# Optimization experiments

Hardware: AMD Instinct MI355X
Metric: run time of the kernel (lower is better)

## Reference

```python
import jax, jax.numpy as jnp
import numpy as np

# dims
B, D, H, W, C = 8, 16, 56, 56, 96
WD, WH, WW = 2, 7, 7          # window size (depth, height, width)
SD, SH, SW = 1, 3, 3          # shift size
NH = 3                        # num heads
HD = C // NH                  # head dim = 32
N = WD * WH * WW              # tokens per window = 98
NW = (D // WD) * (H // WH) * (W // WW)  # windows per image = 512
HIDDEN = 4 * C
EPS = 1e-5
TABLE = (2 * WD - 1) * (2 * WH - 1) * (2 * WW - 1)  # 507


def _rel_pos_index():
    # Faithful replica of get_relative_position_index (note the nonstandard
    # meshgrid argument order: width, depth, height with indexing='ij').
    yy, zz, xx = np.meshgrid(np.arange(WW), np.arange(WD), np.arange(WH), indexing='ij')
    coords = np.stack([zz, yy, xx]).reshape(3, -1)          # [3, N]
    rel = coords[:, :, None] - coords[:, None, :]           # [3, N, N]
    rel = rel.transpose(1, 2, 0)
    z = (rel[..., 0] + WD - 1) * (2 * WH - 1) * (2 * WW - 1)
    x = (rel[..., 1] + WH - 1) * (2 * WW - 1)
    y = rel[..., 2] + WW - 1
    return (z + x + y).astype(np.int32)                     # [N, N], values < 507


def _attn_mask():
    # Standard shifted-window mask: label 3x3x3 regions, -100 where labels differ.
    img = np.zeros((D, H, W), dtype=np.int32)
    cnt = 0
    for ds in (slice(0, -WD), slice(-WD, -SD), slice(-SD, None)):
        for hs in (slice(0, -WH), slice(-WH, -SH), slice(-SH, None)):
            for ws in (slice(0, -WW), slice(-WW, -SW), slice(-SW, None)):
                img[ds, hs, ws] = cnt
                cnt += 1
    mw = img.reshape(D // WD, WD, H // WH, WH, W // WW, WW)
    mw = mw.transpose(0, 2, 4, 1, 3, 5).reshape(NW, N)
    diff = mw[:, None, :] - mw[:, :, None]
    return np.where(diff != 0, np.float32(-100.0), np.float32(0.0))  # [NW, N, N]


def setup_inputs() -> dict:
    key = jax.random.key(0)
    ks = jax.random.split(key, 12)
    s = 0.02
    return {
        "x": jax.random.normal(ks[0], (B, D, H, W, C), jnp.float32),
        "mask_matrix": jnp.asarray(_attn_mask()),
        "g1": jnp.ones((C,), jnp.float32),
        "b1": jnp.zeros((C,), jnp.float32),
        "w_qkv": jax.random.normal(ks[1], (C, 3 * C), jnp.float32) * s,
        "b_qkv": jnp.zeros((3 * C,), jnp.float32),
        "w_proj": jax.random.normal(ks[2], (C, C), jnp.float32) * s,
        "b_proj": jnp.zeros((C,), jnp.float32),
        "bias_table": jax.random.normal(ks[3], (TABLE, NH), jnp.float32) * s,
        "rel_index": jnp.asarray(_rel_pos_index()),
        "g2": jnp.ones((C,), jnp.float32),
        "b2": jnp.zeros((C,), jnp.float32),
        "w_fc1": jax.random.normal(ks[4], (C, HIDDEN), jnp.float32) * s,
        "b_fc1": jnp.zeros((HIDDEN,), jnp.float32),
        "w_fc2": jax.random.normal(ks[5], (HIDDEN, C), jnp.float32) * s,
        "b_fc2": jnp.zeros((C,), jnp.float32),
    }


def _layernorm(x, g, b):
    mu = jnp.mean(x, axis=-1, keepdims=True)
    var = jnp.var(x, axis=-1, keepdims=True)
    return (x - mu) * jax.lax.rsqrt(var + EPS) * g + b


def reference(x, mask_matrix, g1, b1, w_qkv, b_qkv, w_proj, b_proj,
              bias_table, rel_index, g2, b2, w_fc1, b_fc1, w_fc2, b_fc2):
    shortcut = x
    h = _layernorm(x, g1, b1)
    # cyclic shift (no padding needed: dims divisible by window)
    h = jnp.roll(h, shift=(-SD, -SH, -SW), axis=(1, 2, 3))
    # window partition -> [B*NW, N, C]
    xw = h.reshape(B, D // WD, WD, H // WH, WH, W // WW, WW, C)
    xw = xw.transpose(0, 1, 3, 5, 2, 4, 6, 7).reshape(-1, N, C)
    # attention
    qkv = xw @ w_qkv + b_qkv                                   # [BW, N, 3C]
    qkv = qkv.reshape(-1, N, 3, NH, HD).transpose(2, 0, 3, 1, 4)  # [3, BW, NH, N, HD]
    q = qkv[0] * (HD ** -0.5)
    k = qkv[1]
    v = qkv[2]
    attn = jnp.einsum('bhnd,bhmd->bhnm', q, k)                 # [BW, NH, N, N]
    bias = bias_table[rel_index].transpose(2, 0, 1)            # [NH, N, N]
    attn = attn + bias[None]
    attn = attn.reshape(B, NW, NH, N, N) + mask_matrix[None, :, None]
    attn = jax.nn.softmax(attn.reshape(-1, NH, N, N), axis=-1)
    out = jnp.einsum('bhnm,bhmd->bnhd', attn, v).reshape(-1, N, C)
    out = out @ w_proj + b_proj
    # window reverse -> [B, D, H, W, C]
    out = out.reshape(B, D // WD, H // WH, W // WW, WD, WH, WW, C)
    out = out.transpose(0, 1, 4, 2, 5, 3, 6, 7).reshape(B, D, H, W, C)
    out = jnp.roll(out, shift=(SD, SH, SW), axis=(1, 2, 3))
    x = shortcut + out
    # MLP branch
    h2 = _layernorm(x, g2, b2)
    h2 = jax.nn.gelu(h2 @ w_fc1 + b_fc1, approximate=False) @ w_fc2 + b_fc2
    return x + h2
```

## Files before the change

kernel.cpp:

```cpp
#include <hip/hip_runtime.h>
#include <hip/hip_bf16.h>

typedef _Float16 f16x4 __attribute__((ext_vector_type(4)));
typedef _Float16 f16x8 __attribute__((ext_vector_type(8)));
typedef __fp16   h16x2 __attribute__((ext_vector_type(2)));
typedef __fp16   h16x4 __attribute__((ext_vector_type(4)));
typedef float f32x16 __attribute__((ext_vector_type(16)));

#define SCALE_Q 0.17677669529663687f
#define LOG2E   1.44269504088896340f

static __device__ __forceinline__ f16x4 pack4(float a, float b, float c, float d) {
    h16x2 lo = __builtin_amdgcn_cvt_pkrtz(a, b);
    h16x2 hi = __builtin_amdgcn_cvt_pkrtz(c, d);
    h16x4 v = __builtin_shufflevector(lo, hi, 0, 1, 2, 3);
    return __builtin_bit_cast(f16x4, v);
}

static __device__ __forceinline__ float gelu_fast(float v) {
    float z = v * (1.f + 0.044715f * v * v) * 2.3026082f;
    return v * __builtin_amdgcn_rcpf(1.f + __builtin_amdgcn_exp2f(-z));
}

#define WQKVP_OFF  0ull
#define WPP_OFF    55296ull
#define W1P_OFF    73728ull
#define W2P_OFF    147456ull
#define BMT_OFF    221184ull

__global__ __launch_bounds__(256) void k_prep(
    const float* __restrict__ w_qkv, const float* __restrict__ w_proj,
    const float* __restrict__ w_fc1, const float* __restrict__ w_fc2,
    const float* __restrict__ btab, const int* __restrict__ relidx,
    char* __restrict__ ws) {
    _Float16* wqkvp = (_Float16*)(ws + WQKVP_OFF);
    _Float16* wpp   = (_Float16*)(ws + WPP_OFF);
    _Float16* w1p   = (_Float16*)(ws + W1P_OFF);
    _Float16* w2p   = (_Float16*)(ws + W2P_OFF);
    _Float16* bmt   = (_Float16*)(ws + BMT_OFF);
    int e = blockIdx.x * 256 + threadIdx.x;
    if (e < 27648) {
        int ct = e / 3072; int r = e % 3072;
        int c = r >> 9; int l = (r >> 3) & 63; int j = r & 7;
        int k = 16 * c + 8 * (l >> 5) + j, col = ct * 32 + (l & 31);
        wqkvp[e] = (_Float16)w_qkv[k * 288 + col];
    } else if (e < 36864) {
        int r0 = e - 27648;
        int ct = r0 / 3072; int r = r0 % 3072;
        int S = r >> 8; int li = (r >> 2) & 63; int j4 = r & 3;
        int k = 8 * S + 4 * (li >> 5) + j4, col = ct * 32 + (li & 31);
        wpp[r0] = (_Float16)w_proj[k * 96 + col];
    } else if (e < 73728) {
        int r0 = e - 36864;
        int nt = r0 / 3072; int r = r0 % 3072;
        int c = r >> 9; int l = (r >> 3) & 63; int j = r & 7;
        int k = 16 * c + 8 * (l >> 5) + j, col = nt * 32 + (l & 31);
        w1p[r0] = (_Float16)w_fc1[k * 384 + col];
    } else if (e < 110592) {
        int r0 = e - 73728;
        int ct = r0 / 12288; int r = r0 % 12288;
        int c = r >> 9; int l = (r >> 3) & 63; int j = r & 7;
        int k = 16 * c + 8 * (l >> 5) + j, col = ct * 32 + (l & 31);
        w2p[r0] = (_Float16)w_fc2[k * 96 + col];
    } else if (e < 110592 + 235200) {
        int r = e - 110592;
        int cls = r / 29400;
        int r2 = r % 29400;
        int hh = r2 / 9800;
        int ij = r2 % 9800;
        int i = ij / 100, j = ij % 100;
        if (j < 98) {
            int lab[2];
            #pragma unroll
            for (int q = 0; q < 2; ++q) {
                int t = q ? j : i;
                int td = t / 49, rr = t % 49, th = rr / 7, tw = rr % 7;
                int ld = (cls & 4) ? (td == 0 ? 1 : 2) : 0;
                int lh = (cls & 2) ? (th < 4 ? 1 : 2) : 0;
                int lw = (cls & 1) ? (tw < 4 ? 1 : 2) : 0;
                lab[q] = (ld * 3 + lh) * 3 + lw;
            }
            float mask = (lab[0] != lab[1]) ? -100.f : 0.f;
            bmt[r] = (_Float16)((btab[relidx[i * 98 + j] * 3 + hh] + mask) * LOG2E);
        } else {
            bmt[r] = (_Float16)(-30000.f);
        }
    }
}

__global__ __launch_bounds__(256, 4) void k_attn15(
    const float* __restrict__ x,
    const float* __restrict__ g1v, const float* __restrict__ b1v,
    const float* __restrict__ b_qkv, const float* __restrict__ b_proj,
    const char* __restrict__ ws,
    float* __restrict__ out) {
    __shared__ __align__(16) char smem[40864];
    _Float16* xw    = (_Float16*)smem;
    _Float16* VTs   = (_Float16*)smem;
    _Float16* Qs    = (_Float16*)(smem + 20384);
    _Float16* Ks    = (_Float16*)(smem + 30624);
    _Float16* stage = (_Float16*)smem;

    const _Float16* wqkvp = (const _Float16*)(ws + WQKVP_OFF);
    const _Float16* wpp   = (const _Float16*)(ws + WPP_OFF);
    const _Float16* bmt   = (const _Float16*)(ws + BMT_OFF);

    const int tid = threadIdx.x;
    const int w = blockIdx.x;
    const int b = w >> 9, nwi = w & 511;
    const int dq = nwi >> 6, hq = (nwi >> 3) & 7, wq = nwi & 7;
    const int cls = ((dq == 7) << 2) | ((hq == 7) << 1) | (wq == 7);

    {
        const int lane = tid & 31, sub = tid >> 5;
        for (int it = 0; it < 13; ++it) {
            int t = sub + 8 * it;
            if (t < 98) {
                int td = t / 49; int r = t - td * 49; int th = r / 7; int tw = r - th * 7;
                int gd = (dq * 2 + td + 1) & 15;
                int gh = hq * 7 + th + 3; if (gh >= 56) gh -= 56;
                int gw = wq * 7 + tw + 3; if (gw >= 56) gw -= 56;
                const float* row = x + (size_t)(((b * 16 + gd) * 56 + gh) * 56 + gw) * 96;
                float v0 = row[lane], v1 = row[lane + 32], v2 = row[lane + 64];
                float s = v0 + v1 + v2, s2 = v0 * v0 + v1 * v1 + v2 * v2;
                #pragma unroll
                for (int off = 16; off >= 1; off >>= 1) {
                    s  += __shfl_xor(s,  off, 32);
                    s2 += __shfl_xor(s2, off, 32);
                }
                float mu = s * (1.f / 96.f);
                float rs = rsqrtf(s2 * (1.f / 96.f) - mu * mu + 1e-5f);
                xw[t * 104 + lane]      = (_Float16)((v0 - mu) * rs * g1v[lane]      + b1v[lane]);
                xw[t * 104 + lane + 32] = (_Float16)((v1 - mu) * rs * g1v[lane + 32] + b1v[lane + 32]);
                xw[t * 104 + lane + 64] = (_Float16)((v2 - mu) * rs * g1v[lane + 64] + b1v[lane + 64]);
            }
        }
    }
    __syncthreads();

    const int l = tid & 63, wid = tid >> 6, n = l & 31, hi = l >> 5;
    const int mtb = wid * 32;
    const int i_q = mtb + n;
    const bool iv = (i_q < 98);
    const int ir = iv ? i_q : 97;

    f16x8 af[6];
    if (iv) {
        #pragma unroll
        for (int c = 0; c < 6; ++c)
            af[c] = *(const f16x8*)&xw[i_q * 104 + 16 * c + 8 * hi];
    } else {
        #pragma unroll
        for (int c = 0; c < 6; ++c) af[c] = f16x8{0, 0, 0, 0, 0, 0, 0, 0};
    }
    __syncthreads();

    f16x4 ofr[3][4];

    #pragma unroll
    for (int h = 0; h < 3; ++h) {
        #pragma unroll
        for (int sel = 0; sel < 3; ++sel) {
            int ct = sel * 3 + h;
            float bias = b_qkv[sel * 96 + h * 32 + n];
            f32x16 acc;
            #pragma unroll
            for (int r2 = 0; r2 < 16; ++r2) acc[r2] = bias;
            __builtin_amdgcn_s_setprio(1);
            #pragma unroll
            for (int c = 0; c < 6; ++c) {
                f16x8 bf = *(const f16x8*)&wqkvp[((ct * 6 + c) * 64 + l) * 8];
                acc = __builtin_amdgcn_mfma_f32_32x32x16_f16(af[c], bf, acc, 0, 0, 0);
            }
            __builtin_amdgcn_s_setprio(0);
            if (sel == 2) {
                #pragma unroll
                for (int s4 = 0; s4 < 4; ++s4) {
                    f16x4 vv = pack4(acc[4 * s4 + 0], acc[4 * s4 + 1], acc[4 * s4 + 2], acc[4 * s4 + 3]);
                    int t0 = mtb + 8 * s4 + 4 * hi;
                    *(f16x4*)&VTs[n * 140 + t0] = vv;
                }
            } else {
                #pragma unroll
                for (int rg = 0; rg < 16; ++rg) {
                    int t = mtb + (rg & 3) + 8 * (rg >> 2) + 4 * hi;
                    float v = acc[rg];
                    if (sel == 0) Qs[t * 40 + n] = (_Float16)(v * (SCALE_Q * LOG2E));
                    else          Ks[t * 40 + n] = (_Float16)v;
                }
            }
        }
        __syncthreads();

        {
            const _Float16* bmtp = bmt + ((size_t)(cls * 3 + h) * 98 + ir) * 100;
            f32x16 oacc;
            #pragma unroll
            for (int r2 = 0; r2 < 16; ++r2) oacc[r2] = 0.f;
            float ssum = 0.f;
            f16x8 bq[2];
            #pragma unroll
            for (int c = 0; c < 2; ++c)
                bq[c] = *(const f16x8*)&Qs[i_q * 40 + 16 * c + 8 * hi];
            __builtin_amdgcn_s_setprio(1);
            #pragma unroll
            for (int jt = 0; jt < 4; ++jt) {
                f32x16 a;
                #pragma unroll
                for (int rg4 = 0; rg4 < 4; ++rg4) {
                    int j0 = jt * 32 + 8 * rg4 + 4 * hi;
                    int j0c = (j0 < 96) ? j0 : 96;
                    f16x4 bv4 = *(const f16x4*)&bmtp[j0c];
                    bool valid = iv && (j0 < 98);
                    #pragma unroll
                    for (int q = 0; q < 4; ++q)
                        a[rg4 * 4 + q] = valid ? (float)bv4[q] : -1e30f;
                }
                #pragma unroll
                for (int c = 0; c < 2; ++c) {
                    f16x8 ak = *(const f16x8*)&Ks[(jt * 32 + n) * 40 + 16 * c + 8 * hi];
                    a = __builtin_amdgcn_mfma_f32_32x32x16_f16(ak, bq[c], a, 0, 0, 0);
                }
                #pragma unroll
                for (int rg = 0; rg < 16; ++rg) {
                    float p = __builtin_amdgcn_exp2f(a[rg]);
                    a[rg] = p;
                    ssum += p;
                }
                #pragma unroll
                for (int s4 = 0; s4 < 4; ++s4) {
                    f16x4 pf = pack4(a[4 * s4 + 0], a[4 * s4 + 1], a[4 * s4 + 2], a[4 * s4 + 3]);
                    f16x4 av = *(const f16x4*)&VTs[n * 140 + 8 * (jt * 4 + s4) + 4 * hi];
                    oacc = __builtin_amdgcn_mfma_f32_32x32x8f16(av, pf, oacc, 0, 0, 0);
                }
            }
            __builtin_amdgcn_s_setprio(0);
            ssum += __shfl_xor(ssum, 32);
            float inv = 1.f / ssum;
            #pragma unroll
            for (int s4 = 0; s4 < 4; ++s4) {
                ofr[h][s4] = pack4(oacc[4 * s4 + 0] * inv, oacc[4 * s4 + 1] * inv,
                                   oacc[4 * s4 + 2] * inv, oacc[4 * s4 + 3] * inv);
            }
        }
        __syncthreads();
    }

    #pragma unroll
    for (int ct = 0; ct < 3; ++ct) {
        f32x16 acc;
        #pragma unroll
        for (int r2 = 0; r2 < 16; ++r2) acc[r2] = 0.f;
        __builtin_amdgcn_s_setprio(1);
        #pragma unroll
        for (int S = 0; S < 12; ++S) {
            f16x4 aw = *(const f16x4*)&wpp[((ct * 12 + S) * 64 + l) * 4];
            acc = __builtin_amdgcn_mfma_f32_32x32x8f16(aw, ofr[S >> 2][S & 3], acc, 0, 0, 0);
        }
        __builtin_amdgcn_s_setprio(0);
        if (iv) {
            #pragma unroll
            for (int s4 = 0; s4 < 4; ++s4) {
                f16x4 sv = pack4(acc[4 * s4 + 0], acc[4 * s4 + 1], acc[4 * s4 + 2], acc[4 * s4 + 3]);
                int col0 = ct * 32 + 8 * s4 + 4 * hi;
                *(f16x4*)&stage[i_q * 100 + col0] = sv;
            }
        }
    }
    __syncthreads();
    for (int e = tid; e < 2352; e += 256) {
        int t = e / 24, q4 = (e - (e / 24) * 24) * 4;
        int td = t / 49; int r = t - td * 49; int th = r / 7; int tw = r - th * 7;
        int gd = (dq * 2 + td + 1) & 15;
        int gh = hq * 7 + th + 3; if (gh >= 56) gh -= 56;
        int gw = wq * 7 + tw + 3; if (gw >= 56) gw -= 56;
        size_t base = (size_t)(((b * 16 + gd) * 56 + gh) * 56 + gw) * 96 + q4;
        float4 xv = *(const float4*)&x[base];
        float4 bp = *(const float4*)&b_proj[q4];
        f16x4 sv = *(const f16x4*)&stage[t * 100 + q4];
        float4 ov;
        ov.x = xv.x + bp.x + (float)sv[0];
        ov.y = xv.y + bp.y + (float)sv[1];
        ov.z = xv.z + bp.z + (float)sv[2];
        ov.w = xv.w + bp.w + (float)sv[3];
        *(float4*)&out[base] = ov;
    }
}

__global__ __launch_bounds__(256, 5) void k_mlp6(
    const float* __restrict__ g2v, const float* __restrict__ b2v,
    const float* __restrict__ b_fc1, const float* __restrict__ b_fc2,
    const char* __restrict__ ws,
    float* __restrict__ out) {
    __shared__ __align__(16) _Float16 xb[32 * 104];
    __shared__ __align__(16) _Float16 hb[32 * 392];
    const _Float16* w1p = (const _Float16*)(ws + W1P_OFF);
    const _Float16* w2p = (const _Float16*)(ws + W2P_OFF);
    const int tid = threadIdx.x;
    const size_t tokBase = (size_t)blockIdx.x * 32;
    {
        const int lane = tid & 31, sub = tid >> 5;
        #pragma unroll
        for (int it = 0; it < 4; ++it) {
            int rt = sub + 8 * it;
            const float* row = out + (tokBase + rt) * 96;
            float v0 = row[lane], v1 = row[lane + 32], v2 = row[lane + 64];
            float s = v0 + v1 + v2, s2 = v0 * v0 + v1 * v1 + v2 * v2;
            #pragma unroll
            for (int off = 16; off >= 1; off >>= 1) {
                s  += __shfl_xor(s,  off, 32);
                s2 += __shfl_xor(s2, off, 32);
            }
            float mu = s * (1.f / 96.f);
            float rs = rsqrtf(s2 * (1.f / 96.f) - mu * mu + 1e-5f);
            xb[rt * 104 + lane]      = (_Float16)((v0 - mu) * rs * g2v[lane]      + b2v[lane]);
            xb[rt * 104 + lane + 32] = (_Float16)((v1 - mu) * rs * g2v[lane + 32] + b2v[lane + 32]);
            xb[rt * 104 + lane + 64] = (_Float16)((v2 - mu) * rs * g2v[lane + 64] + b2v[lane + 64]);
        }
    }
    __syncthreads();
    const int l = tid & 63, wid = tid >> 6, n = l & 31, hi = l >> 5;
    {
        f16x8 af[6];
        #pragma unroll
        for (int c = 0; c < 6; ++c)
            af[c] = *(const f16x8*)&xb[n * 104 + 16 * c + 8 * hi];
        #pragma unroll
        for (int s3 = 0; s3 < 3; ++s3) {
            int nt = wid + 4 * s3;
            float bias = b_fc1[nt * 32 + n];
            f32x16 acc;
            #pragma unroll
            for (int r2 = 0; r2 < 16; ++r2) acc[r2] = bias;
            __builtin_amdgcn_s_setprio(1);
            #pragma unroll
            for (int c = 0; c < 6; ++c) {
                f16x8 bf = *(const f16x8*)&w1p[((nt * 6 + c) * 64 + l) * 8];
                acc = __builtin_amdgcn_mfma_f32_32x32x16_f16(af[c], bf, acc, 0, 0, 0);
            }
            __builtin_amdgcn_s_setprio(0);
            #pragma unroll
            for (int rg = 0; rg < 16; ++rg) {
                int t = (rg & 3) + 8 * (rg >> 2) + 4 * hi;
                hb[t * 392 + nt * 32 + n] = (_Float16)gelu_fast(acc[rg]);
            }
        }
    }
    __syncthreads();
    if (wid < 3) {
        int ct = wid;
        float bias = b_fc2[ct * 32 + n];
        f32x16 acc;
        #pragma unroll
        for (int r2 = 0; r2 < 16; ++r2) acc[r2] = bias;
        __builtin_amdgcn_s_setprio(1);
        #pragma unroll
        for (int c = 0; c < 24; ++c) {
            f16x8 ah = *(const f16x8*)&hb[n * 392 + 16 * c + 8 * hi];
            f16x8 bf = *(const f16x8*)&w2p[((ct * 24 + c) * 64 + l) * 8];
            acc = __builtin_amdgcn_mfma_f32_32x32x16_f16(ah, bf, acc, 0, 0, 0);
        }
        __builtin_amdgcn_s_setprio(0);
        #pragma unroll
        for (int rg = 0; rg < 16; ++rg) {
            int t = (rg & 3) + 8 * (rg >> 2) + 4 * hi;
            size_t idx = (tokBase + t) * 96 + ct * 32 + n;
            out[idx] = out[idx] + acc[rg];
        }
    }
}

extern "C" void kernel_launch(void* const* d_in, const int* in_sizes, int n_in,
                              void* d_out, int out_size, void* d_ws, size_t ws_size,
                              hipStream_t stream) {
    const float* x      = (const float*)d_in[0];
    const float* g1     = (const float*)d_in[2];
    const float* b1     = (const float*)d_in[3];
    const float* w_qkv  = (const float*)d_in[4];
    const float* b_qkv  = (const float*)d_in[5];
    const float* w_proj = (const float*)d_in[6];
    const float* b_proj = (const float*)d_in[7];
    const float* btab   = (const float*)d_in[8];
    const int*   relidx = (const int*)d_in[9];
    const float* g2     = (const float*)d_in[10];
    const float* b2     = (const float*)d_in[11];
    const float* w_fc1  = (const float*)d_in[12];
    const float* b_fc1  = (const float*)d_in[13];
    const float* w_fc2  = (const float*)d_in[14];
    const float* b_fc2  = (const float*)d_in[15];
    float* out = (float*)d_out;
    char*  ws  = (char*)d_ws;

    hipLaunchKernelGGL(k_prep, dim3(1351), dim3(256), 0, stream,
                       w_qkv, w_proj, w_fc1, w_fc2, btab, relidx, ws);
    hipLaunchKernelGGL(k_attn15, dim3(4096), dim3(256), 0, stream,
                       x, g1, b1, b_qkv, b_proj, (const char*)ws, out);
    hipLaunchKernelGGL(k_mlp6, dim3(401408 / 32), dim3(256), 0, stream,
                       g2, b2, b_fc1, b_fc2, (const char*)ws, out);
}
```

Measured before the change: 329.0 us.

## Fuse MLP branch into window attention kernel, chunking hidden dim through LDS

Merges the separate MLP kernel into the attention kernel. Each window block computes the residual, LayerNorm2, FC1+GELU and FC2 for its 98 tokens, streaming the 384-wide hidden layer in four 96-column chunks through shared memory and accumulating FC2 in registers. This avoids re-reading the intermediate activations from global memory and one kernel launch. In exchange it adds register pressure from three extra accumulators, wastes MFMA work on padded rows (98 tokens padded to 128), and does a read-modify-write of the output in a scattered shifted-window order.

```diff
diff --git a/kernel.cpp b/kernel.cpp
--- a/kernel.cpp
+++ b/kernel.cpp
@@ -88,21 +88,28 @@
     }
 }
 
-__global__ __launch_bounds__(256, 4) void k_attn15(
+__global__ __launch_bounds__(256, 4) void k_fused(
     const float* __restrict__ x,
     const float* __restrict__ g1v, const float* __restrict__ b1v,
     const float* __restrict__ b_qkv, const float* __restrict__ b_proj,
+    const float* __restrict__ g2v, const float* __restrict__ b2v,
+    const float* __restrict__ b_fc1, const float* __restrict__ b_fc2,
     const char* __restrict__ ws,
     float* __restrict__ out) {
-    __shared__ __align__(16) char smem[40864];
+    __shared__ __align__(16) char smem[40960];
     _Float16* xw    = (_Float16*)smem;
     _Float16* VTs   = (_Float16*)smem;
     _Float16* Qs    = (_Float16*)(smem + 20384);
     _Float16* Ks    = (_Float16*)(smem + 30624);
     _Float16* stage = (_Float16*)smem;
+    _Float16* xb    = (_Float16*)smem;
+    _Float16* hb    = (_Float16*)(smem + 21632);
+    unsigned* rowbase = (unsigned*)(smem + 40448);
 
     const _Float16* wqkvp = (const _Float16*)(ws + WQKVP_OFF);
     const _Float16* wpp   = (const _Float16*)(ws + WPP_OFF);
+    const _Float16* w1p   = (const _Float16*)(ws + W1P_OFF);
+    const _Float16* w2p   = (const _Float16*)(ws + W2P_OFF);
     const _Float16* bmt   = (const _Float16*)(ws + BMT_OFF);
 
     const int tid = threadIdx.x;
@@ -263,71 +270,60 @@
             for (int s4 = 0; s4 < 4; ++s4) {
                 f16x4 sv = pack4(acc[4 * s4 + 0], acc[4 * s4 + 1], acc[4 * s4 + 2], acc[4 * s4 + 3]);
                 int col0 = ct * 32 + 8 * s4 + 4 * hi;
-                *(f16x4*)&stage[i_q * 100 + col0] = sv;
+                *(f16x4*)&stage[i_q * 104 + col0] = sv;
             }
         }
     }
     __syncthreads();
-    for (int e = tid; e < 2352; e += 256) {
-        int t = e / 24, q4 = (e - (e / 24) * 24) * 4;
-        int td = t / 49; int r = t - td * 49; int th = r / 7; int tw = r - th * 7;
-        int gd = (dq * 2 + td + 1) & 15;
-        int gh = hq * 7 + th + 3; if (gh >= 56) gh -= 56;
-        int gw = wq * 7 + tw + 3; if (gw >= 56) gw -= 56;
-        size_t base = (size_t)(((b * 16 + gd) * 56 + gh) * 56 + gw) * 96 + q4;
-        float4 xv = *(const float4*)&x[base];
-        float4 bp = *(const float4*)&b_proj[q4];
-        f16x4 sv = *(const f16x4*)&stage[t * 100 + q4];
-        float4 ov;
-        ov.x = xv.x + bp.x + (float)sv[0];
-        ov.y = xv.y + bp.y + (float)sv[1];
-        ov.z = xv.z + bp.z + (float)sv[2];
-        ov.w = xv.w + bp.w + (float)sv[3];
-        *(float4*)&out[base] = ov;
-    }
-}
-
-__global__ __launch_bounds__(256, 5) void k_mlp6(
-    const float* __restrict__ g2v, const float* __restrict__ b2v,
-    const float* __restrict__ b_fc1, const float* __restrict__ b_fc2,
-    const char* __restrict__ ws,
-    float* __restrict__ out) {
-    __shared__ __align__(16) _Float16 xb[32 * 104];
-    __shared__ __align__(16) _Float16 hb[32 * 392];
-    const _Float16* w1p = (const _Float16*)(ws + W1P_OFF);
-    const _Float16* w2p = (const _Float16*)(ws + W2P_OFF);
-    const int tid = threadIdx.x;
-    const size_t tokBase = (size_t)blockIdx.x * 32;
+
     {
         const int lane = tid & 31, sub = tid >> 5;
-        #pragma unroll
-        for (int it = 0; it < 4; ++it) {
-            int rt = sub + 8 * it;
-            const float* row = out + (tokBase + rt) * 96;
-            float v0 = row[lane], v1 = row[lane + 32], v2 = row[lane + 64];
-            float s = v0 + v1 + v2, s2 = v0 * v0 + v1 * v1 + v2 * v2;
-            #pragma unroll
-            for (int off = 16; off >= 1; off >>= 1) {
-                s  += __shfl_xor(s,  off, 32);
-                s2 += __shfl_xor(s2, off, 32);
-            }
-            float mu = s * (1.f / 96.f);
-            float rs = rsqrtf(s2 * (1.f / 96.f) - mu * mu + 1e-5f);
-            xb[rt * 104 + lane]      = (_Float16)((v0 - mu) * rs * g2v[lane]      + b2v[lane]);
-            xb[rt * 104 + lane + 32] = (_Float16)((v1 - mu) * rs * g2v[lane + 32] + b2v[lane + 32]);
-            xb[rt * 104 + lane + 64] = (_Float16)((v2 - mu) * rs * g2v[lane + 64] + b2v[lane + 64]);
+        for (int it = 0; it < 13; ++it) {
+            int t = sub + 8 * it;
+            if (t < 98) {
+                int td = t / 49; int r = t - td * 49; int th = r / 7; int tw = r - th * 7;
+                int gd = (dq * 2 + td + 1) & 15;
+                int gh = hq * 7 + th + 3; if (gh >= 56) gh -= 56;
+                int gw = wq * 7 + tw + 3; if (gw >= 56) gw -= 56;
+                unsigned base = (unsigned)((((b * 16 + gd) * 56 + gh) * 56 + gw) * 96);
+                if (lane == 0) rowbase[t] = base;
+                float v0 = x[base + lane]      + b_proj[lane]      + (float)stage[t * 104 + lane];
+                float v1 = x[base + lane + 32] + b_proj[lane + 32] + (float)stage[t * 104 + lane + 32];
+                float v2 = x[base + lane + 64] + b_proj[lane + 64] + (float)stage[t * 104 + lane + 64];
+                out[base + lane]      = v0;
+                out[base + lane + 32] = v1;
+                out[base + lane + 64] = v2;
+                float s = v0 + v1 + v2, s2 = v0 * v0 + v1 * v1 + v2 * v2;
+                #pragma unroll
+                for (int off = 16; off >= 1; off >>= 1) {
+                    s  += __shfl_xor(s,  off, 32);
+                    s2 += __shfl_xor(s2, off, 32);
+                }
+                float mu = s * (1.f / 96.f);
+                float rs = rsqrtf(s2 * (1.f / 96.f) - mu * mu + 1e-5f);
+                xb[t * 104 + lane]      = (_Float16)((v0 - mu) * rs * g2v[lane]      + b2v[lane]);
+                xb[t * 104 + lane + 32] = (_Float16)((v1 - mu) * rs * g2v[lane + 32] + b2v[lane + 32]);
+                xb[t * 104 + lane + 64] = (_Float16)((v2 - mu) * rs * g2v[lane + 64] + b2v[lane + 64]);
+            }
         }
     }
     __syncthreads();
-    const int l = tid & 63, wid = tid >> 6, n = l & 31, hi = l >> 5;
-    {
-        f16x8 af[6];
-        #pragma unroll
-        for (int c = 0; c < 6; ++c)
-            af[c] = *(const f16x8*)&xb[n * 104 + 16 * c + 8 * hi];
-        #pragma unroll
-        for (int s3 = 0; s3 < 3; ++s3) {
-            int nt = wid + 4 * s3;
+
+    const int rowA = mtb + n;
+    const int rowc = (rowA < 98) ? rowA : 97;
+    f16x8 axb[6];
+    #pragma unroll
+    for (int c = 0; c < 6; ++c)
+        axb[c] = *(const f16x8*)&xb[rowc * 104 + 16 * c + 8 * hi];
+    f32x16 macc0, macc1, macc2;
+    #pragma unroll
+    for (int r2 = 0; r2 < 16; ++r2) { macc0[r2] = 0.f; macc1[r2] = 0.f; macc2[r2] = 0.f; }
+
+    #pragma unroll
+    for (int qq = 0; qq < 4; ++qq) {
+        #pragma unroll
+        for (int s = 0; s < 3; ++s) {
+            int nt = qq * 3 + s;
             float bias = b_fc1[nt * 32 + n];
             f32x16 acc;
             #pragma unroll
@@ -336,36 +332,40 @@
             #pragma unroll
             for (int c = 0; c < 6; ++c) {
                 f16x8 bf = *(const f16x8*)&w1p[((nt * 6 + c) * 64 + l) * 8];
-                acc = __builtin_amdgcn_mfma_f32_32x32x16_f16(af[c], bf, acc, 0, 0, 0);
+                acc = __builtin_amdgcn_mfma_f32_32x32x16_f16(axb[c], bf, acc, 0, 0, 0);
             }
             __builtin_amdgcn_s_setprio(0);
             #pragma unroll
             for (int rg = 0; rg < 16; ++rg) {
-                int t = (rg & 3) + 8 * (rg >> 2) + 4 * hi;
-                hb[t * 392 + nt * 32 + n] = (_Float16)gelu_fast(acc[rg]);
-            }
-        }
-    }
-    __syncthreads();
-    if (wid < 3) {
-        int ct = wid;
-        float bias = b_fc2[ct * 32 + n];
-        f32x16 acc;
-        #pragma unroll
-        for (int r2 = 0; r2 < 16; ++r2) acc[r2] = bias;
+                int t = mtb + (rg & 3) + 8 * (rg >> 2) + 4 * hi;
+                if (t < 98) hb[t * 96 + s * 32 + n] = (_Float16)gelu_fast(acc[rg]);
+            }
+        }
         __builtin_amdgcn_s_setprio(1);
         #pragma unroll
-        for (int c = 0; c < 24; ++c) {
-            f16x8 ah = *(const f16x8*)&hb[n * 392 + 16 * c + 8 * hi];
-            f16x8 bf = *(const f16x8*)&w2p[((ct * 24 + c) * 64 + l) * 8];
-            acc = __builtin_amdgcn_mfma_f32_32x32x16_f16(ah, bf, acc, 0, 0, 0);
+        for (int c2 = 0; c2 < 6; ++c2) {
+            f16x8 ah = *(const f16x8*)&hb[rowc * 96 + 16 * c2 + 8 * hi];
+            f16x8 bf0 = *(const f16x8*)&w2p[((0 * 24 + qq * 6 + c2) * 64 + l) * 8];
+            f16x8 bf1 = *(const f16x8*)&w2p[((1 * 24 + qq * 6 + c2) * 64 + l) * 8];
+            f16x8 bf2 = *(const f16x8*)&w2p[((2 * 24 + qq * 6 + c2) * 64 + l) * 8];
+            macc0 = __builtin_amdgcn_mfma_f32_32x32x16_f16(ah, bf0, macc0, 0, 0, 0);
+            macc1 = __builtin_amdgcn_mfma_f32_32x32x16_f16(ah, bf1, macc1, 0, 0, 0);
+            macc2 = __builtin_amdgcn_mfma_f32_32x32x16_f16(ah, bf2, macc2, 0, 0, 0);
         }
         __builtin_amdgcn_s_setprio(0);
+    }
+
+    {
+        float bb0 = b_fc2[n], bb1 = b_fc2[32 + n], bb2 = b_fc2[64 + n];
         #pragma unroll
         for (int rg = 0; rg < 16; ++rg) {
-            int t = (rg & 3) + 8 * (rg >> 2) + 4 * hi;
-            size_t idx = (tokBase + t) * 96 + ct * 32 + n;
-            out[idx] = out[idx] + acc[rg];
+            int t = mtb + (rg & 3) + 8 * (rg >> 2) + 4 * hi;
+            if (t < 98) {
+                unsigned base = rowbase[t];
+                out[base + n]      += macc0[rg] + bb0;
+                out[base + 32 + n] += macc1[rg] + bb1;
+                out[base + 64 + n] += macc2[rg] + bb2;
+            }
         }
     }
 }
@@ -393,8 +393,7 @@
 
     hipLaunchKernelGGL(k_prep, dim3(1351), dim3(256), 0, stream,
                        w_qkv, w_proj, w_fc1, w_fc2, btab, relidx, ws);
-    hipLaunchKernelGGL(k_attn15, dim3(4096), dim3(256), 0, stream,
-                       x, g1, b1, b_qkv, b_proj, (const char*)ws, out);
-    hipLaunchKernelGGL(k_mlp6, dim3(401408 / 32), dim3(256), 0, stream,
-                       g2, b2, b_fc1, b_fc2, (const char*)ws, out);
-}
+    hipLaunchKernelGGL(k_fused, dim3(4096), dim3(256), 0, stream,
+                       x, g1, b1, b_qkv, b_proj, g2, b2, b_fc1, b_fc2,
+                       (const char*)ws, out);
+}
```

New measurement: 473.7 us. +44.0%, slower.
